# Performance work log

Measured on AMD Instinct MI355X. Metric: run time of the kernel, lower is better.

## Reference

```python
import jax, jax.numpy as jnp
from jax import lax
import numpy as np

POINT_PAIRS = 10000
SIGMA = 0.03
ALPHA = 1.0
MIN_DEPTH = -0.001
MAX_DEPTH = 80.0


def _get_edges(images):
    # images: [n,3,H,W]; Sobel on channel 0, VALID conv then zero-pad by 1 (as in torch code)
    x = images[:, :1]
    kx = jnp.array([[-1., 0., 1.], [-2., 0., 2.], [-1., 0., 1.]], jnp.float32).reshape(1, 1, 3, 3)
    ky = jnp.array([[1., 2., 1.], [0., 0., 0.], [-1., -2., -1.]], jnp.float32).reshape(1, 1, 3, 3)
    gx = lax.conv_general_dilated(x, kx, (1, 1), 'VALID')
    gy = lax.conv_general_dilated(x, ky, (1, 1), 'VALID')
    edges = jnp.sqrt(gx * gx + gy * gy)
    thetas = jnp.arctan2(gy, gx)
    pad = ((0, 0), (0, 0), (1, 1), (1, 1))
    return jnp.pad(edges, pad), jnp.pad(thetas, pad)


def _sample_and_loss(key, inp, tgt, edge, theta, smask):
    # inp/tgt/edge/theta: [H,W] float; smask: [H,W] bool
    H, W = inp.shape
    k1, k2, k3 = jax.random.split(key, 3)
    # edge-guided anchor sampling: uniform over {edge >= 0.1*max} & strict_mask, with replacement
    emask = (edge >= 0.1 * edge.max()) & smask
    p = emask.reshape(-1).astype(jnp.float32)
    p = p / jnp.maximum(p.sum(), 1.0)
    flat_idx = jax.random.choice(k1, H * W, (POINT_PAIRS,), replace=True, p=p)
    sh = flat_idx // W
    sw = flat_idx % W
    th = theta.reshape(-1)[flat_idx]
    # signed step distances along / perpendicular to the edge direction
    dist = jax.random.randint(k2, (4, POINT_PAIRS), 2, 31).astype(jnp.float32)
    sign = jnp.array([-1., -1., 1., 1.], jnp.float32).reshape(4, 1)
    dist = dist * sign
    # random_direct: p<0.5 -> along gradient; else rotate theta by pi/2 (swapped cos/sin)
    pdir = jax.random.uniform(k3) < 0.5
    th2 = ((th + jnp.pi / 2) + jnp.pi) % (2 * jnp.pi) - jnp.pi
    col1 = sw[None, :] + jnp.round(dist * jnp.cos(th)[None, :]).astype(jnp.int32)
    row1 = sh[None, :] + jnp.round(dist * jnp.sin(th)[None, :]).astype(jnp.int32)
    col2 = sw[None, :] + jnp.round(dist * jnp.sin(th2)[None, :]).astype(jnp.int32)
    row2 = sh[None, :] + jnp.round(dist * jnp.cos(th2)[None, :]).astype(jnp.int32)
    col = jnp.where(pdir, col1, col2)  # [4,N]
    row = jnp.where(pdir, row1, row2)
    inb = (col >= 0) & (col <= W - 1) & (row >= 0) & (row <= H - 1)
    valid = jnp.all(inb, axis=0)  # [N]; torch drops these columns, we mask instead
    colc = jnp.clip(col, 0, W - 1)
    rowc = jnp.clip(row, 0, H - 1)
    # pairs (a,b),(b,c),(c,d) -> A = [a,b,c], B = [b,c,d]
    rA = jnp.concatenate([rowc[0], rowc[1], rowc[2]])
    cA = jnp.concatenate([colc[0], colc[1], colc[2]])
    rB = jnp.concatenate([rowc[1], rowc[2], rowc[3]])
    cB = jnp.concatenate([colc[1], colc[2], colc[3]])
    vm = jnp.concatenate([valid, valid, valid]).astype(jnp.float32)  # [3N]
    iA = inp[rA, cA]
    iB = inp[rB, cB]
    tA = tgt[rA, cA]
    tB = tgt[rB, cB]
    # ranking loss
    ratio = (tA + 1e-6) / (tB + 1e-6)
    absdiff = jnp.abs(tA - tB)
    maxdiff = jnp.max(jnp.where(vm > 0, absdiff, 0.0))
    tw = jnp.exp(absdiff / (maxdiff + 1e-6))
    eq = (ratio < 1.0 + SIGMA) & (ratio > 1.0 / (1.0 + SIGMA))
    labels = jnp.where(ratio >= 1.0 + SIGMA, 1.0,
                       jnp.where(ratio <= 1.0 / (1.0 + SIGMA), -1.0, 0.0))
    equal_loss = (iA - iB) ** 2 / tw * eq.astype(jnp.float32)
    unequal_loss = jnp.log1p(jnp.exp((iB - iA) * labels)) * (1.0 - eq.astype(jnp.float32))
    cnt = jnp.maximum(vm.sum(), 1.0)
    loss = ALPHA * jnp.sum(equal_loss * vm) / cnt + jnp.sum(unequal_loss * vm) / cnt
    return loss, vm.sum()


def setup_inputs() -> dict:
    key = jax.random.key(0)
    k1, k2, k3, k4 = jax.random.split(key, 4)
    n, H, W = 8, 1024, 1024
    inputs = jax.random.normal(k1, (n, 1, H, W), jnp.float32)
    targets = jax.random.uniform(k2, (n, 1, H, W), jnp.float32)
    images = jax.random.uniform(k3, (n, 3, H, W), jnp.float32)
    depth_gt = jax.random.uniform(k4, (n, 1, H, W), jnp.float32)
    return {"inputs": inputs, "targets": targets, "images": images, "depth_gt": depth_gt}


def reference(inputs, targets, images, depth_gt):
    n = inputs.shape[0]
    strict = (depth_gt > MIN_DEPTH) & (depth_gt < MAX_DEPTH) & ~(targets == 80.0)
    edges, thetas = _get_edges(images)
    keys = jax.random.split(jax.random.key(42), n)
    losses, counts = jax.vmap(_sample_and_loss)(
        keys, inputs[:, 0], targets[:, 0], edges[:, 0], thetas[:, 0], strict[:, 0])
    return losses.sum() / n, counts.sum() / n
```

## Files before the change

kernel.cpp:

```cpp
#include <hip/hip_runtime.h>
#include <math.h>
#include <stdint.h>

#define NIMG 8
#define HH 1024
#define WW 1024
#define NPIX (HH*WW)
#define PAIRS 10000
#define STRIP 8
#define NSTRIPS 128
#define S1BLOCKS 40
#define WSLOTS (S1BLOCKS*4)
#define FBLK 4
#define QPAIRS (PAIRS/FBLK)

#define OFF_EDGE 0
#define OFF_MD   1024
#define OFF_RES  4096
#define OFF_CTR  4112

__device__ __forceinline__ uint64_t mix64(uint64_t x){
    x += 0x9E3779B97F4A7C15ull;
    x = (x ^ (x >> 30)) * 0xBF58476D1CE4E5B9ull;
    x = (x ^ (x >> 27)) * 0x94D049BB133111EBull;
    return x ^ (x >> 31);
}

__device__ __forceinline__ float block_reduce_max(float v, float* sm){
    for (int off = 32; off; off >>= 1)
        v = fmaxf(v, __shfl_down(v, off));
    int wv = threadIdx.x >> 6, lane = threadIdx.x & 63;
    int nw = blockDim.x >> 6;
    if (lane == 0) sm[wv] = v;
    __syncthreads();
    if (threadIdx.x == 0){
        float m = sm[0];
        for (int i = 1; i < nw; ++i) m = fmaxf(m, sm[i]);
        sm[0] = m;
    }
    __syncthreads();
    float r = sm[0];
    __syncthreads();
    return r;
}

__device__ __forceinline__ float block_reduce_sum(float v, float* sm){
    for (int off = 32; off; off >>= 1)
        v += __shfl_down(v, off);
    int wv = threadIdx.x >> 6, lane = threadIdx.x & 63;
    int nw = blockDim.x >> 6;
    if (lane == 0) sm[wv] = v;
    __syncthreads();
    if (threadIdx.x == 0){
        float m = sm[0];
        for (int i = 1; i < nw; ++i) m += sm[i];
        sm[0] = m;
    }
    __syncthreads();
    float r = sm[0];
    __syncthreads();
    return r;
}

__device__ __forceinline__ void sobel_at(const float* __restrict__ x, int r, int c,
                                         float& gx, float& gy){
    const float* p0 = x + (size_t)(r-1)*WW + c;
    const float* p1 = x + (size_t)r*WW + c;
    const float* p2 = x + (size_t)(r+1)*WW + c;
    float a = p0[-1], b = p0[0], cc = p0[1];
    float d = p1[-1],             e = p1[1];
    float f = p2[-1], g = p2[0], h = p2[1];
    gx = (cc - a) + 2.0f*(e - d) + (h - f);
    gy = (a + 2.0f*b + cc) - (f + 2.0f*g + h);
}

__device__ __forceinline__ void load16(const float* __restrict__ p, float* d){
    const float4* q = (const float4*)p;
    float4 v0 = q[0], v1 = q[1], v2 = q[2], v3 = q[3];
    d[0]=v0.x; d[1]=v0.y; d[2]=v0.z; d[3]=v0.w;
    d[4]=v1.x; d[5]=v1.y; d[6]=v1.z; d[7]=v1.w;
    d[8]=v2.x; d[9]=v2.y; d[10]=v2.z; d[11]=v2.w;
    d[12]=v3.x; d[13]=v3.y; d[14]=v3.z; d[15]=v3.w;
}

__global__ __launch_bounds__(256) void edgemax_kernel(const float* __restrict__ images,
                                                      float* __restrict__ ws){
    if (blockIdx.x == 0 && blockIdx.y == 0 && threadIdx.x < 17)
        ws[OFF_RES + threadIdx.x] = 0.0f;

    int img  = blockIdx.y;
    const float* x = images + (size_t)img * 3 * NPIX;
    int wv   = threadIdx.x >> 6;
    int lane = threadIdx.x & 63;
    int strip = blockIdx.x * 4 + wv;
    int r0 = 1 + strip * STRIP;
    int r1 = min(r0 + STRIP - 1, HH - 2);
    int c0 = lane * 16;

    float a[16], b[16], n[16];
    load16(x + (size_t)(r0-1)*WW + c0, a);
    load16(x + (size_t)r0*WW + c0, b);

    float m = 0.0f;
    for (int r = r0; r <= r1; ++r){
        load16(x + (size_t)(r+1)*WW + c0, n);
        float sx[16], dy[16];
        #pragma unroll
        for (int i = 0; i < 16; ++i){
            sx[i] = a[i] + 2.0f*b[i] + n[i];
            dy[i] = a[i] - n[i];
        }
        float sxl = __shfl_up(sx[15], 1);
        float sxr = __shfl_down(sx[0], 1);
        float dyl = __shfl_up(dy[15], 1);
        float dyr = __shfl_down(dy[0], 1);
        #pragma unroll
        for (int j = 0; j < 16; ++j){
            float sl = (j == 0)  ? sxl : sx[j-1];
            float sr = (j == 15) ? sxr : sx[j+1];
            float dl = (j == 0)  ? dyl : dy[j-1];
            float dr = (j == 15) ? dyr : dy[j+1];
            float gx = sr - sl;
            float gy = dl + 2.0f*dy[j] + dr;
            float e2 = gx*gx + gy*gy;
            int c = c0 + j;
            if (c >= 1 && c <= WW-2) m = fmaxf(m, e2);
        }
        #pragma unroll
        for (int i = 0; i < 16; ++i){ a[i] = b[i]; b[i] = n[i]; }
    }
    for (int off = 32; off; off >>= 1)
        m = fmaxf(m, __shfl_down(m, off));
    if (lane == 0)
        ws[OFF_EDGE + img * NSTRIPS + strip] = m;
}

__global__ __launch_bounds__(256) void sample_kernel(
                               const float* __restrict__ inputs,
                               const float* __restrict__ targets,
                               const float* __restrict__ images,
                               const float* __restrict__ depth_gt,
                               float* __restrict__ ws,
                               float4* __restrict__ recsA,
                               float4* __restrict__ recsB){
    __shared__ float sred[4];
    int img = blockIdx.y;
    int jb  = blockIdx.x;
    int tid = threadIdx.x;
    int j   = jb * 256 + tid;
    const float* x   = images   + (size_t)img * 3 * NPIX;
    const float* inp = inputs   + (size_t)img * NPIX;
    const float* tgt = targets  + (size_t)img * NPIX;
    const float* dgt = depth_gt + (size_t)img * NPIX;

    float ev = 0.0f;
    if (tid < NSTRIPS) ev = ws[OFF_EDGE + img * NSTRIPS + tid];
    float thr2 = 0.01f * block_reduce_max(ev, sred);

    float mdiff = 0.0f;
    float4 recA = make_float4(0.f, 0.f, 0.f, 0.f);
    float4 recB = make_float4(0.f, 0.f, 0.f, 0.f);

    if (j < PAIRS){
        uint64_t base = ((uint64_t)(img * PAIRS + j)) << 10;
        bool pdir = (mix64(((uint64_t)(NIMG * PAIRS + img)) << 10) & 1ull) != 0ull;

        int sh = -1, sw = -1;
        float gxs = 0.f, gys = 0.f, e2s = 1.f;
        for (int att = 0; att < 900; ++att){
            uint64_t u = mix64(base + (uint64_t)att);
            uint32_t pix = (uint32_t)(u >> 44);
            int r = (int)(pix >> 10);
            int c = (int)(pix & (WW - 1));
            if (r == 0 || r >= HH-1 || c == 0 || c >= WW-1) continue;
            float gx, gy;
            sobel_at(x, r, c, gx, gy);
            float e2 = gx*gx + gy*gy;
            if (!(e2 >= thr2)) continue;
            float dg = dgt[r*WW + c];
            float tg = tgt[r*WW + c];
            if (!(dg > -0.001f && dg < 80.0f && tg != 80.0f)) continue;
            sh = r; sw = c; gxs = gx; gys = gy; e2s = e2;
            break;
        }

        if (sh >= 0){
            float inv = rsqrtf(e2s);
            float cmul = gxs * inv;
            float rmul = gys * inv;
            if (!pdir) cmul = -cmul;

            uint64_t u0 = mix64(base + 1000ull);
            uint64_t u1 = mix64(base + 1001ull);
            float dist[4];
            dist[0] = -(float)(2u + (uint32_t)(u0 & 0xFFFFFFFFull) % 29u);
            dist[1] = -(float)(2u + (uint32_t)(u0 >> 32) % 29u);
            dist[2] =  (float)(2u + (uint32_t)(u1 & 0xFFFFFFFFull) % 29u);
            dist[3] =  (float)(2u + (uint32_t)(u1 >> 32) % 29u);

            int rowc[4], colc[4];
            bool valid = true;
            #pragma unroll
            for (int k = 0; k < 4; ++k){
                int cc2 = sw + (int)rintf(dist[k] * cmul);
                int rr2 = sh + (int)rintf(dist[k] * rmul);
                if (cc2 < 0 || cc2 > WW-1 || rr2 < 0 || rr2 > HH-1) valid = false;
                colc[k] = min(max(cc2, 0), WW-1);
                rowc[k] = min(max(rr2, 0), HH-1);
            }

            if (valid){
                float t4[4], i4[4];
                #pragma unroll
                for (int k = 0; k < 4; ++k){
                    int p = rowc[k]*WW + colc[k];
                    t4[k] = tgt[p];
                    i4[k] = inp[p];
                }
                float d2a[3], ada[3];
                float un = 0.0f;
                #pragma unroll
                for (int k = 0; k < 3; ++k){
                    float tA = t4[k], tB = t4[k+1];
                    float ratio = (tA + 1e-6f) / (tB + 1e-6f);
                    float adk = fabsf(tA - tB);
                    mdiff = fmaxf(mdiff, adk);
                    bool eq = (ratio < 1.03f) && (ratio > 0.9708737864077669f);
                    if (eq){
                        float d = i4[k] - i4[k+1];
                        d2a[k] = d*d; ada[k] = adk;
                    } else {
                        d2a[k] = 0.f; ada[k] = 0.f;
                        float lab = (ratio >= 1.03f) ? 1.0f : -1.0f;
                        un += log1pf(expf((i4[k+1] - i4[k]) * lab));
                    }
                }
                recA = make_float4(d2a[0], d2a[1], d2a[2], un);
                recB = make_float4(ada[0], ada[1], ada[2], 3.0f);
            }
        }
        recsA[img * PAIRS + j] = recA;
        recsB[img * PAIRS + j] = recB;
    }

    for (int off = 32; off; off >>= 1)
        mdiff = fmaxf(mdiff, __shfl_down(mdiff, off));
    if ((tid & 63) == 0)
        ws[OFF_MD + img * WSLOTS + jb*4 + (tid >> 6)] = mdiff;
}

__global__ __launch_bounds__(256) void finish_kernel(
                               float* __restrict__ ws,
                               const float4* __restrict__ recsA,
                               const float4* __restrict__ recsB,
                               float* __restrict__ out){
    __shared__ float sred[4];
    __shared__ unsigned lastflag;
    int img = blockIdx.x >> 2;
    int q   = blockIdx.x & 3;
    int tid = threadIdx.x;

    float mv = 0.0f;
    if (tid < WSLOTS) mv = ws[OFF_MD + img * WSLOTS + tid];
    float md = block_reduce_max(mv, sred);
    float inv = 1.0f / (md + 1e-6f);

    float loss = 0.0f, cnt = 0.0f;
    int base = img * PAIRS + q * QPAIRS;
    for (int r = tid; r < QPAIRS; r += 256){
        float4 A = recsA[base + r];
        float4 B = recsB[base + r];
        loss += A.w
              + A.x * expf(-B.x * inv)
              + A.y * expf(-B.y * inv)
              + A.z * expf(-B.z * inv);
        cnt  += B.w;
    }
    loss = block_reduce_sum(loss, sred);
    cnt  = block_reduce_sum(cnt, sred);

    if (tid == 0){
        atomicAdd(&ws[OFF_RES + img*2 + 0], loss);
        atomicAdd(&ws[OFF_RES + img*2 + 1], cnt);
        __threadfence();
        unsigned old = atomicAdd((unsigned int*)&ws[OFF_CTR], 1u);
        lastflag = (old == (unsigned)(NIMG*FBLK - 1)) ? 1u : 0u;
    }
    __syncthreads();

    if (lastflag){
        __threadfence();
        float val = 0.0f, cv = 0.0f;
        if (tid < NIMG){
            float li = atomicAdd(&ws[OFF_RES + tid*2 + 0], 0.0f);
            float ci = atomicAdd(&ws[OFF_RES + tid*2 + 1], 0.0f);
            val = li / fmaxf(ci, 1.0f);
            cv  = ci;
        }
        for (int off = 4; off; off >>= 1){
            val += __shfl_down(val, off);
            cv  += __shfl_down(cv,  off);
        }
        if (tid == 0){
            out[0] = val / (float)NIMG;
            out[1] = cv  / (float)NIMG;
        }
    }
}

extern "C" void kernel_launch(void* const* d_in, const int* in_sizes, int n_in,
                              void* d_out, int out_size, void* d_ws, size_t ws_size,
                              hipStream_t stream) {
    const float* inputs  = (const float*)d_in[0];
    const float* targets = (const float*)d_in[1];
    const float* images  = (const float*)d_in[2];
    const float* depth   = (const float*)d_in[3];
    float* out = (float*)d_out;

    float* ws     = (float*)d_ws;
    float4* recsA = (float4*)((char*)d_ws + 65536);
    float4* recsB = recsA + (size_t)NIMG * PAIRS;

    hipLaunchKernelGGL(edgemax_kernel, dim3(NSTRIPS/4, NIMG), dim3(256), 0, stream,
                       images, ws);
    hipLaunchKernelGGL(sample_kernel, dim3(S1BLOCKS, NIMG), dim3(256), 0, stream,
                       inputs, targets, images, depth, ws, recsA, recsB);
    hipLaunchKernelGGL(finish_kernel, dim3(NIMG*FBLK), dim3(256), 0, stream,
                       ws, recsA, recsB, out);
}
```

Before: 44.41 us.

## Fuse finish into sample kernel with per-image last-block reduction and compacted segments

Removes the separate finish kernel launch. The sample kernel now reduces the unequal loss and count in-block and tracks the max diff with an atomicMax. It compacts only the equal-pair records into a per-image segment buffer using ballot/popcount. The last block per image then applies the exp weighting and the last image finalises the output. This saves a launch and the dense record write/read, at the cost of atomics, a serialized tail done by one block per image, and counters that rely on the zeroing in edgemax_kernel.

```diff
diff --git a/kernel.cpp b/kernel.cpp
--- a/kernel.cpp
+++ b/kernel.cpp
@@ -10,14 +10,15 @@
 #define STRIP 8
 #define NSTRIPS 128
 #define S1BLOCKS 40
-#define WSLOTS (S1BLOCKS*4)
-#define FBLK 4
-#define QPAIRS (PAIRS/FBLK)
+#define SEGCAP 30720
 
 #define OFF_EDGE 0
-#define OFF_MD   1024
 #define OFF_RES  4096
-#define OFF_CTR  4112
+#define OFF_MDI  4112
+#define OFF_DONE 4120
+#define OFF_IMGD 4128
+#define OFF_SEGC 4136
+#define ZERO_N   48
 
 __device__ __forceinline__ uint64_t mix64(uint64_t x){
     x += 0x9E3779B97F4A7C15ull;
@@ -30,14 +31,10 @@
     for (int off = 32; off; off >>= 1)
         v = fmaxf(v, __shfl_down(v, off));
     int wv = threadIdx.x >> 6, lane = threadIdx.x & 63;
-    int nw = blockDim.x >> 6;
     if (lane == 0) sm[wv] = v;
     __syncthreads();
-    if (threadIdx.x == 0){
-        float m = sm[0];
-        for (int i = 1; i < nw; ++i) m = fmaxf(m, sm[i]);
-        sm[0] = m;
-    }
+    if (threadIdx.x == 0)
+        sm[0] = fmaxf(fmaxf(sm[0], sm[1]), fmaxf(sm[2], sm[3]));
     __syncthreads();
     float r = sm[0];
     __syncthreads();
@@ -48,14 +45,10 @@
     for (int off = 32; off; off >>= 1)
         v += __shfl_down(v, off);
     int wv = threadIdx.x >> 6, lane = threadIdx.x & 63;
-    int nw = blockDim.x >> 6;
     if (lane == 0) sm[wv] = v;
     __syncthreads();
-    if (threadIdx.x == 0){
-        float m = sm[0];
-        for (int i = 1; i < nw; ++i) m += sm[i];
-        sm[0] = m;
-    }
+    if (threadIdx.x == 0)
+        sm[0] = sm[0] + sm[1] + sm[2] + sm[3];
     __syncthreads();
     float r = sm[0];
     __syncthreads();
@@ -85,7 +78,7 @@
 
 __global__ __launch_bounds__(256) void edgemax_kernel(const float* __restrict__ images,
                                                       float* __restrict__ ws){
-    if (blockIdx.x == 0 && blockIdx.y == 0 && threadIdx.x < 17)
+    if (blockIdx.x == 0 && blockIdx.y == 0 && threadIdx.x < ZERO_N)
         ws[OFF_RES + threadIdx.x] = 0.0f;
 
     int img  = blockIdx.y;
@@ -135,19 +128,21 @@
         ws[OFF_EDGE + img * NSTRIPS + strip] = m;
 }
 
-__global__ __launch_bounds__(256) void sample_kernel(
+__global__ __launch_bounds__(256) void sample_finish_kernel(
                                const float* __restrict__ inputs,
                                const float* __restrict__ targets,
                                const float* __restrict__ images,
                                const float* __restrict__ depth_gt,
                                float* __restrict__ ws,
-                               float4* __restrict__ recsA,
-                               float4* __restrict__ recsB){
+                               float2* __restrict__ segs,
+                               float* __restrict__ out){
     __shared__ float sred[4];
-    int img = blockIdx.y;
-    int jb  = blockIdx.x;
-    int tid = threadIdx.x;
-    int j   = jb * 256 + tid;
+    __shared__ unsigned flag1, flag2;
+    int img  = blockIdx.y;
+    int jb   = blockIdx.x;
+    int tid  = threadIdx.x;
+    int lane = tid & 63;
+    int j    = jb * 256 + tid;
     const float* x   = images   + (size_t)img * 3 * NPIX;
     const float* inp = inputs   + (size_t)img * NPIX;
     const float* tgt = targets  + (size_t)img * NPIX;
@@ -157,9 +152,9 @@
     if (tid < NSTRIPS) ev = ws[OFF_EDGE + img * NSTRIPS + tid];
     float thr2 = 0.01f * block_reduce_max(ev, sred);
 
-    float mdiff = 0.0f;
-    float4 recA = make_float4(0.f, 0.f, 0.f, 0.f);
-    float4 recB = make_float4(0.f, 0.f, 0.f, 0.f);
+    float mdiff = 0.0f, un = 0.0f, cntv = 0.0f;
+    float d2a[3] = {0.f,0.f,0.f}, ada[3] = {0.f,0.f,0.f};
+    bool  eqf[3] = {false,false,false};
 
     if (j < PAIRS){
         uint64_t base = ((uint64_t)(img * PAIRS + j)) << 10;
@@ -217,8 +212,6 @@
                     t4[k] = tgt[p];
                     i4[k] = inp[p];
                 }
-                float d2a[3], ada[3];
-                float un = 0.0f;
                 #pragma unroll
                 for (int k = 0; k < 3; ++k){
                     float tA = t4[k], tB = t4[k+1];
@@ -228,82 +221,85 @@
                     bool eq = (ratio < 1.03f) && (ratio > 0.9708737864077669f);
                     if (eq){
                         float d = i4[k] - i4[k+1];
-                        d2a[k] = d*d; ada[k] = adk;
+                        d2a[k] = d*d; ada[k] = adk; eqf[k] = true;
                     } else {
-                        d2a[k] = 0.f; ada[k] = 0.f;
                         float lab = (ratio >= 1.03f) ? 1.0f : -1.0f;
                         un += log1pf(expf((i4[k+1] - i4[k]) * lab));
                     }
                 }
-                recA = make_float4(d2a[0], d2a[1], d2a[2], un);
-                recB = make_float4(ada[0], ada[1], ada[2], 3.0f);
-            }
-        }
-        recsA[img * PAIRS + j] = recA;
-        recsB[img * PAIRS + j] = recB;
-    }
-
-    for (int off = 32; off; off >>= 1)
-        mdiff = fmaxf(mdiff, __shfl_down(mdiff, off));
-    if ((tid & 63) == 0)
-        ws[OFF_MD + img * WSLOTS + jb*4 + (tid >> 6)] = mdiff;
-}
-
-__global__ __launch_bounds__(256) void finish_kernel(
-                               float* __restrict__ ws,
-                               const float4* __restrict__ recsA,
-                               const float4* __restrict__ recsB,
-                               float* __restrict__ out){
-    __shared__ float sred[4];
-    __shared__ unsigned lastflag;
-    int img = blockIdx.x >> 2;
-    int q   = blockIdx.x & 3;
-    int tid = threadIdx.x;
-
-    float mv = 0.0f;
-    if (tid < WSLOTS) mv = ws[OFF_MD + img * WSLOTS + tid];
-    float md = block_reduce_max(mv, sred);
-    float inv = 1.0f / (md + 1e-6f);
-
-    float loss = 0.0f, cnt = 0.0f;
-    int base = img * PAIRS + q * QPAIRS;
-    for (int r = tid; r < QPAIRS; r += 256){
-        float4 A = recsA[base + r];
-        float4 B = recsB[base + r];
-        loss += A.w
-              + A.x * expf(-B.x * inv)
-              + A.y * expf(-B.y * inv)
-              + A.z * expf(-B.z * inv);
-        cnt  += B.w;
-    }
-    loss = block_reduce_sum(loss, sred);
-    cnt  = block_reduce_sum(cnt, sred);
-
+                cntv = 3.0f;
+            }
+        }
+    }
+
+    {
+        unsigned long long m0 = __ballot(eqf[0]);
+        unsigned long long m1 = __ballot(eqf[1]);
+        unsigned long long m2 = __ballot(eqf[2]);
+        int c0 = __popcll(m0), c1 = __popcll(m1), c2 = __popcll(m2);
+        int wavetot = c0 + c1 + c2;
+        unsigned basei = 0;
+        if (lane == 0 && wavetot)
+            basei = atomicAdd((unsigned int*)&ws[OFF_SEGC + img], (unsigned)wavetot);
+        basei = (unsigned)__shfl((int)basei, 0);
+        unsigned long long below = (lane == 63) ? ~0ull >> 1 : ((1ull << lane) - 1ull);
+        below = (1ull << lane) - 1ull;
+        float2* sp = segs + (size_t)img * SEGCAP;
+        if (eqf[0]) sp[basei + __popcll(m0 & below)]           = make_float2(d2a[0], ada[0]);
+        if (eqf[1]) sp[basei + c0 + __popcll(m1 & below)]      = make_float2(d2a[1], ada[1]);
+        if (eqf[2]) sp[basei + c0 + c1 + __popcll(m2 & below)] = make_float2(d2a[2], ada[2]);
+    }
+
+    float mdb = block_reduce_max(mdiff, sred);
+    float unb = block_reduce_sum(un, sred);
+    float cnb = block_reduce_sum(cntv, sred);
     if (tid == 0){
-        atomicAdd(&ws[OFF_RES + img*2 + 0], loss);
-        atomicAdd(&ws[OFF_RES + img*2 + 1], cnt);
+        if (mdb > 0.0f) atomicMax((unsigned int*)&ws[OFF_MDI + img], __float_as_uint(mdb));
+        atomicAdd(&ws[OFF_RES + img*2 + 0], unb);
+        atomicAdd(&ws[OFF_RES + img*2 + 1], cnb);
         __threadfence();
-        unsigned old = atomicAdd((unsigned int*)&ws[OFF_CTR], 1u);
-        lastflag = (old == (unsigned)(NIMG*FBLK - 1)) ? 1u : 0u;
-    }
-    __syncthreads();
-
-    if (lastflag){
+        unsigned old = atomicAdd((unsigned int*)&ws[OFF_DONE + img], 1u);
+        flag1 = (old == (unsigned)(S1BLOCKS - 1)) ? 1u : 0u;
+    }
+    __syncthreads();
+
+    if (flag1){
         __threadfence();
-        float val = 0.0f, cv = 0.0f;
-        if (tid < NIMG){
-            float li = atomicAdd(&ws[OFF_RES + tid*2 + 0], 0.0f);
-            float ci = atomicAdd(&ws[OFF_RES + tid*2 + 1], 0.0f);
-            val = li / fmaxf(ci, 1.0f);
-            cv  = ci;
-        }
-        for (int off = 4; off; off >>= 1){
-            val += __shfl_down(val, off);
-            cv  += __shfl_down(cv,  off);
-        }
+        float md = __uint_as_float(atomicAdd((unsigned int*)&ws[OFF_MDI + img], 0u));
+        float inv = 1.0f / (md + 1e-6f);
+        unsigned nseg = atomicAdd((unsigned int*)&ws[OFF_SEGC + img], 0u);
+        const float2* sp = segs + (size_t)img * SEGCAP;
+        float eqs = 0.0f;
+        for (unsigned r = tid; r < nseg; r += 256){
+            float2 s = sp[r];
+            eqs += s.x * expf(-s.y * inv);
+        }
+        eqs = block_reduce_sum(eqs, sred);
         if (tid == 0){
-            out[0] = val / (float)NIMG;
-            out[1] = cv  / (float)NIMG;
+            atomicAdd(&ws[OFF_RES + img*2 + 0], eqs);
+            __threadfence();
+            unsigned o2 = atomicAdd((unsigned int*)&ws[OFF_IMGD], 1u);
+            flag2 = (o2 == (unsigned)(NIMG - 1)) ? 1u : 0u;
+        }
+        __syncthreads();
+
+        if (flag2){
+            __threadfence();
+            float val = 0.0f, cv = 0.0f;
+            if (tid < NIMG){
+                float li = atomicAdd(&ws[OFF_RES + tid*2 + 0], 0.0f);
+                float ci = atomicAdd(&ws[OFF_RES + tid*2 + 1], 0.0f);
+                val = li / fmaxf(ci, 1.0f);
+                cv  = ci;
+            }
+            for (int off = 4; off; off >>= 1){
+                val += __shfl_down(val, off);
+                cv  += __shfl_down(cv,  off);
+            }
+            if (tid == 0){
+                out[0] = val / (float)NIMG;
+                out[1] = cv  / (float)NIMG;
+            }
         }
     }
 }
@@ -317,14 +313,11 @@
     const float* depth   = (const float*)d_in[3];
     float* out = (float*)d_out;
 
-    float* ws     = (float*)d_ws;
-    float4* recsA = (float4*)((char*)d_ws + 65536);
-    float4* recsB = recsA + (size_t)NIMG * PAIRS;
+    float* ws    = (float*)d_ws;
+    float2* segs = (float2*)((char*)d_ws + 65536);
 
     hipLaunchKernelGGL(edgemax_kernel, dim3(NSTRIPS/4, NIMG), dim3(256), 0, stream,
                        images, ws);
-    hipLaunchKernelGGL(sample_kernel, dim3(S1BLOCKS, NIMG), dim3(256), 0, stream,
-                       inputs, targets, images, depth, ws, recsA, recsB);
-    hipLaunchKernelGGL(finish_kernel, dim3(NIMG*FBLK), dim3(256), 0, stream,
-                       ws, recsA, recsB, out);
-}
+    hipLaunchKernelGGL(sample_finish_kernel, dim3(S1BLOCKS, NIMG), dim3(256), 0, stream,
+                       inputs, targets, images, depth, ws, segs, out);
+}
```

After: 58.50 us. 1.32x slower.
